# Kernel tuning notes

Measured on AMD Instinct MI355X. Metric: run time of the kernel, lower is better.

The kernel has to match this reference:

```python
import jax, jax.numpy as jnp
import numpy as np

N_NODES = 100000
N_EDGES = 3200000
IN_DIM, HID_DIM, LAT_DIM = 6, 32, 16


def gcn_conv(x, src, dst, W, b, num_nodes):
    """PyG-style GCNConv: add self-loops, symmetric deg^{-1/2} norm, linear, scatter-add.
    src/dst already include self-loops."""
    h = x @ W  # [N, out_dim] -- transform before propagate (small dims)
    ones = jnp.ones(src.shape[0], dtype=x.dtype)
    deg = jax.ops.segment_sum(ones, dst, num_segments=num_nodes)  # in-degree incl. self-loop
    dinv = jax.lax.rsqrt(jnp.maximum(deg, 1.0))
    norm = dinv[src] * dinv[dst]  # [E]
    msg = h[src] * norm[:, None]  # [E, out_dim] -- dominant memory traffic
    out = jax.ops.segment_sum(msg, dst, num_segments=num_nodes)
    return out + b


def setup_inputs() -> dict:
    key = jax.random.key(0)
    k1, k2, k3, k4 = jax.random.split(key, 4)
    x = jax.random.normal(k1, (N_NODES, IN_DIM), dtype=jnp.float32)
    edge_index = jax.random.randint(k2, (2, N_EDGES), 0, N_NODES, dtype=jnp.int64)
    # Glorot-ish init for weights, zeros for biases (PyG GCNConv defaults)
    W1 = jax.random.normal(k3, (IN_DIM, HID_DIM), dtype=jnp.float32) / np.sqrt(IN_DIM)
    b1 = jnp.zeros((HID_DIM,), dtype=jnp.float32)
    W2 = jax.random.normal(k4, (HID_DIM, LAT_DIM), dtype=jnp.float32) / np.sqrt(HID_DIM)
    b2 = jnp.zeros((LAT_DIM,), dtype=jnp.float32)
    return {"x": x, "edge_index": edge_index, "W1": W1, "b1": b1, "W2": W2, "b2": b2}


def reference(x, edge_index, W1, b1, W2, b2):
    num_nodes = x.shape[0]
    loops = jnp.arange(num_nodes, dtype=edge_index.dtype)
    src = jnp.concatenate([edge_index[0], loops])
    dst = jnp.concatenate([edge_index[1], loops])
    h = gcn_conv(x, src, dst, W1, b1, num_nodes)
    h = jax.nn.relu(h)
    # dropout is identity in eval mode (reference baseline)
    z = gcn_conv(h, src, dst, W2, b2, num_nodes)
    return z
```

## Files before the change

kernel.cpp:

```cpp
#include <hip/hip_runtime.h>
#include <hip/hip_fp16.h>

#define N_NODES 100000
#define N_EDGES 3200000
#define IN_DIM 6
#define HID_DIM 32
#define LAT_DIM 16

#define NPB 128
#define NB 782
#define CAP 4800
#define AB_BLOCKS 512
#define CH ((N_EDGES + AB_BLOCKS - 1) / AB_BLOCKS)
#define PL_T 512
#define LP2_CAP 2560

__global__ void k_init(int* __restrict__ bcur) {
    int i = blockIdx.x * blockDim.x + threadIdx.x;
    if (i < NB) bcur[i] = i * CAP;
}

__global__ void __launch_bounds__(PL_T) k_bplace(const int* __restrict__ src,
                                                 const int* __restrict__ dst,
                                                 int* __restrict__ bcur,
                                                 int* __restrict__ bedge, int E) {
    __shared__ int hist[NB];
    __shared__ int lbase[NB];
    __shared__ int gbase[NB];
    __shared__ int cur[NB];
    __shared__ int part[PL_T];
    __shared__ int stage[CH];
    __shared__ unsigned short sbkt[CH];
    int t = threadIdx.x;
    for (int i = t; i < NB; i += PL_T) { hist[i] = 0; cur[i] = 0; }
    __syncthreads();
    int beg = blockIdx.x * CH, end = min(beg + CH, E);
    int nv = (end - beg) >> 1;
    const int2* dst2 = (const int2*)(dst + beg);
    const long long* src2 = (const long long*)(src + beg);
    for (int i = t; i < nv; i += PL_T) {
        int2 d = dst2[i];
        atomicAdd(&hist[d.x >> 7], 1);
        atomicAdd(&hist[d.y >> 7], 1);
    }
    if (((end - beg) & 1) && t == 0) atomicAdd(&hist[dst[end - 1] >> 7], 1);
    __syncthreads();
    int i0 = 2 * t;
    int a = (i0 < NB) ? hist[i0] : 0;
    int b = (i0 + 1 < NB) ? hist[i0 + 1] : 0;
    part[t] = a + b;
    __syncthreads();
    for (int off = 1; off < PL_T; off <<= 1) {
        int v = (t >= off) ? part[t - off] : 0;
        __syncthreads();
        part[t] += v;
        __syncthreads();
    }
    int ex = (t == 0) ? 0 : part[t - 1];
    if (i0 < NB) lbase[i0] = ex;
    if (i0 + 1 < NB) lbase[i0 + 1] = ex + a;
    __syncthreads();
    for (int i = t; i < NB; i += PL_T)
        gbase[i] = hist[i] ? atomicAdd(&bcur[i], hist[i]) : 0;
    __syncthreads();
    for (int i = t; i < nv; i += PL_T) {
        int2 d = dst2[i];
        long long sv = __builtin_nontemporal_load(src2 + i);
        int s0 = (int)(sv & 0xFFFFFFFFLL);
        int s1 = (int)(sv >> 32);
        int bkt0 = d.x >> 7;
        int r0 = atomicAdd(&cur[bkt0], 1);
        int pos0 = lbase[bkt0] + r0;
        stage[pos0] = (s0 << 7) | (d.x & (NPB - 1));
        sbkt[pos0] = (unsigned short)bkt0;
        int bkt1 = d.y >> 7;
        int r1 = atomicAdd(&cur[bkt1], 1);
        int pos1 = lbase[bkt1] + r1;
        stage[pos1] = (s1 << 7) | (d.y & (NPB - 1));
        sbkt[pos1] = (unsigned short)bkt1;
    }
    if (((end - beg) & 1) && t == 0) {
        int d = dst[end - 1], s = src[end - 1];
        int bkt = d >> 7;
        int r = atomicAdd(&cur[bkt], 1);
        int pos = lbase[bkt] + r;
        stage[pos] = (s << 7) | (d & (NPB - 1));
        sbkt[pos] = (unsigned short)bkt;
    }
    __syncthreads();
    int total = end - beg;
    for (int j = t; j < total; j += PL_T) {
        int bkt = sbkt[j];
        bedge[gbase[bkt] + (j - lbase[bkt])] = stage[j];
    }
}

__global__ void __launch_bounds__(256) k_sort(const int* __restrict__ bcur,
                                              const int* __restrict__ bedge,
                                              const float* __restrict__ x,
                                              int2* __restrict__ rowse,
                                              int* __restrict__ perm,
                                              float* __restrict__ dinv,
                                              __half* __restrict__ xs, int N) {
    int b = blockIdx.x;
    __shared__ int cnt[NPB], base[NPB], cur[NPB], scn[NPB];
    __shared__ float dvs[NPB];
    __shared__ int pstage[CAP];
    int t = threadIdx.x;
    if (t < NPB) cnt[t] = 0;
    __syncthreads();
    int beg = b * CAP, end = bcur[b];
    int m = end - beg;
    for (int k = t; k < m; k += blockDim.x)
        atomicAdd(&cnt[bedge[beg + k] & (NPB - 1)], 1);
    __syncthreads();
    if (t < NPB) scn[t] = cnt[t];
    __syncthreads();
    for (int off = 1; off < NPB; off <<= 1) {
        int v = 0;
        if (t < NPB && t >= off) v = scn[t - off];
        __syncthreads();
        if (t < NPB) scn[t] += v;
        __syncthreads();
    }
    if (t < NPB) {
        int ex = scn[t] - cnt[t];
        base[t] = ex;
        cur[t] = 0;
        int node = (b << 7) + t;
        if (node < N) {
            float dv = rsqrtf((float)(cnt[t] + 1));
            dvs[t] = dv;
            dinv[node] = dv;
            rowse[node] = make_int2(beg + ex, beg + ex + cnt[t]);
        }
    }
    __syncthreads();
    for (int k = t; k < m; k += blockDim.x) {
        int w = bedge[beg + k];
        int dl = w & (NPB - 1);
        int pos = base[dl] + atomicAdd(&cur[dl], 1);
        pstage[pos] = w >> 7;
    }
    __syncthreads();
    for (int k = t; k < m; k += blockDim.x)
        perm[beg + k] = pstage[k];
    for (int i = t; i < NPB * 4; i += blockDim.x) {
        int nl = i >> 2, d2 = (i & 3) * 2;
        int node = (b << 7) + nl;
        if (node < N) {
            float dv = dvs[nl];
            float v0 = (d2 < IN_DIM) ? x[(size_t)node * IN_DIM + d2] * dv : 0.f;
            float v1 = (d2 + 1 < IN_DIM) ? x[(size_t)node * IN_DIM + d2 + 1] * dv : 0.f;
            *(__half2*)(xs + (size_t)node * 8 + d2) = __floats2half2_rn(v0, v1);
        }
    }
}

__global__ void __launch_bounds__(256) k_agg1f(const int2* __restrict__ rowse,
                                               const int* __restrict__ perm,
                                               const __half* __restrict__ xs,
                                               const float* __restrict__ dinv,
                                               const float* __restrict__ b1,
                                               const float* __restrict__ W1,
                                               const float* __restrict__ W2,
                                               __half* __restrict__ h2s, int N) {
    __shared__ float w1[IN_DIM * HID_DIM];
    __shared__ float w2[HID_DIM * LAT_DIM];
    __shared__ float bsh[HID_DIM];
    __shared__ float ash[64][HID_DIM + 1];
    __shared__ float y[64][9];
    __shared__ int lperm[LP2_CAP];
    int t = threadIdx.x;
    for (int i = t; i < IN_DIM * HID_DIM; i += 256) w1[i] = W1[i];
    for (int i = t; i < HID_DIM * LAT_DIM; i += 256) w2[i] = W2[i];
    if (t < HID_DIM) bsh[t] = b1[t];
    int nl = t >> 2, p = t & 3;
    int n0 = blockIdx.x * 64;
    int node = n0 + nl;
    int nlast = min(n0 + 63, N - 1);
    int gbeg = rowse[n0].x;
    int gend = rowse[nlast].y;
    int m = gend - gbeg;
    bool valid = (node <= nlast);
    int2 se = valid ? rowse[node] : make_int2(gbeg, gbeg);
    float2 acc = make_float2(0.f, 0.f);
    if (m <= LP2_CAP) {
        for (int i = t; i < m; i += 256) lperm[i] = perm[gbeg + i];
        __syncthreads();
        int k = se.x - gbeg, lend = se.y - gbeg;
        for (; k + 16 <= lend; k += 16) {
            int ss[16];
#pragma unroll
            for (int j = 0; j < 16; j++) ss[j] = lperm[k + j];
            __half2 gg[16];
#pragma unroll
            for (int j = 0; j < 16; j++)
                gg[j] = *(const __half2*)(xs + (size_t)ss[j] * 8 + p * 2);
            float px = 0.f, py = 0.f;
#pragma unroll
            for (int j = 0; j < 16; j++) {
                float2 f = __half22float2(gg[j]);
                px += f.x; py += f.y;
            }
            acc.x += px; acc.y += py;
        }
        for (; k < lend; ++k) {
            float2 f = __half22float2(*(const __half2*)(xs + (size_t)lperm[k] * 8 + p * 2));
            acc.x += f.x; acc.y += f.y;
        }
    } else {
        __syncthreads();
        for (int k = se.x; k < se.y; ++k) {
            float2 f = __half22float2(*(const __half2*)(xs + (size_t)perm[k] * 8 + p * 2));
            acc.x += f.x; acc.y += f.y;
        }
    }
    if (valid) {
        float2 f = __half22float2(*(const __half2*)(xs + (size_t)node * 8 + p * 2));
        y[nl][2 * p] = acc.x + f.x;
        y[nl][2 * p + 1] = acc.y + f.y;
    }
    __syncthreads();
    if (valid) {
        float dv = dinv[node];
        float yy[IN_DIM];
#pragma unroll
        for (int k2 = 0; k2 < IN_DIM; k2++) yy[k2] = y[nl][k2];
        int c0 = p * 8;
#pragma unroll
        for (int q = 0; q < 8; q++) {
            float z = 0.f;
#pragma unroll
            for (int k2 = 0; k2 < IN_DIM; k2++) z += yy[k2] * w1[k2 * HID_DIM + c0 + q];
            ash[nl][c0 + q] = fmaxf(dv * z + bsh[c0 + q], 0.f);
        }
    }
    __syncthreads();
    if (valid) {
        float dv = dinv[node];
        int c = p * 4;
        float z0 = 0.f, z1 = 0.f, z2 = 0.f, z3 = 0.f;
#pragma unroll
        for (int k2 = 0; k2 < HID_DIM; k2++) {
            float a = ash[nl][k2];
            z0 += a * w2[k2 * LAT_DIM + c];
            z1 += a * w2[k2 * LAT_DIM + c + 1];
            z2 += a * w2[k2 * LAT_DIM + c + 2];
            z3 += a * w2[k2 * LAT_DIM + c + 3];
        }
        __half2 h0 = __floats2half2_rn(dv * z0, dv * z1);
        __half2 h1 = __floats2half2_rn(dv * z2, dv * z3);
        uint2 u;
        u.x = *(unsigned*)&h0;
        u.y = *(unsigned*)&h1;
        *(uint2*)(h2s + (size_t)node * LAT_DIM + c) = u;
    }
}

__global__ void __launch_bounds__(256) k_agg2(const int2* __restrict__ rowse,
                                              const int* __restrict__ perm,
                                              const __half* __restrict__ h2s,
                                              const float* __restrict__ dinv,
                                              const float* __restrict__ b2,
                                              float* __restrict__ out, int N) {
    __shared__ int lperm[LP2_CAP];
    int t = threadIdx.x;
    int n0 = blockIdx.x * 64;
    int node = n0 + (t >> 2), p = t & 3;
    int nlast = min(n0 + 63, N - 1);
    int gbeg = rowse[n0].x;
    int gend = rowse[nlast].y;
    int m = gend - gbeg;
    int2 se = (node <= nlast) ? rowse[node] : make_int2(gbeg, gbeg);
    float4 acc = make_float4(0.f, 0.f, 0.f, 0.f);
    if (m <= LP2_CAP) {
        for (int i = t; i < m; i += 256) lperm[i] = perm[gbeg + i];
        __syncthreads();
        int k = se.x - gbeg, lend = se.y - gbeg;
        for (; k + 16 <= lend; k += 16) {
            int ss[16];
#pragma unroll
            for (int j = 0; j < 16; j++) ss[j] = lperm[k + j];
            uint2 gg[16];
#pragma unroll
            for (int j = 0; j < 16; j++)
                gg[j] = *(const uint2*)(h2s + (size_t)ss[j] * LAT_DIM + p * 4);
#pragma unroll
            for (int j = 0; j < 16; j++) {
                float2 f0 = __half22float2(*(const __half2*)&gg[j].x);
                float2 f1 = __half22float2(*(const __half2*)&gg[j].y);
                acc.x += f0.x; acc.y += f0.y; acc.z += f1.x; acc.w += f1.y;
            }
        }
        for (; k < lend; ++k) {
            uint2 g = *(const uint2*)(h2s + (size_t)lperm[k] * LAT_DIM + p * 4);
            float2 f0 = __half22float2(*(const __half2*)&g.x);
            float2 f1 = __half22float2(*(const __half2*)&g.y);
            acc.x += f0.x; acc.y += f0.y; acc.z += f1.x; acc.w += f1.y;
        }
    } else {
        __syncthreads();
        for (int k = se.x; k < se.y; ++k) {
            uint2 g = *(const uint2*)(h2s + (size_t)perm[k] * LAT_DIM + p * 4);
            float2 f0 = __half22float2(*(const __half2*)&g.x);
            float2 f1 = __half22float2(*(const __half2*)&g.y);
            acc.x += f0.x; acc.y += f0.y; acc.z += f1.x; acc.w += f1.y;
        }
    }
    if (node < N) {
        uint2 hh = *(const uint2*)(h2s + (size_t)node * LAT_DIM + p * 4);
        float2 h0 = __half22float2(*(const __half2*)&hh.x);
        float2 h1 = __half22float2(*(const __half2*)&hh.y);
        float dv = dinv[node];
        float4 bb = *(const float4*)(b2 + p * 4);
        float4 o;
        o.x = dv * (acc.x + h0.x) + bb.x;
        o.y = dv * (acc.y + h0.y) + bb.y;
        o.z = dv * (acc.z + h1.x) + bb.z;
        o.w = dv * (acc.w + h1.y) + bb.w;
        *(float4*)(out + (size_t)node * LAT_DIM + p * 4) = o;
    }
}

extern "C" void kernel_launch(void* const* d_in, const int* in_sizes, int n_in,
                              void* d_out, int out_size, void* d_ws, size_t ws_size,
                              hipStream_t stream) {
    const float* x  = (const float*)d_in[0];
    const int*   ei = (const int*)d_in[1];
    const float* W1 = (const float*)d_in[2];
    const float* b1 = (const float*)d_in[3];
    const float* W2 = (const float*)d_in[4];
    const float* b2 = (const float*)d_in[5];
    float* out = (float*)d_out;

    const int N = N_NODES, E = N_EDGES;
    const int* src = ei;
    const int* dst = ei + E;

    char* ws = (char*)d_ws;
    size_t off = 0;
    auto take = [&](size_t bytes) -> void* {
        void* p = ws + off;
        off += (bytes + 255) & ~(size_t)255;
        return p;
    };
    int*    bcur  = (int*)take((size_t)NB * 4);
    int*    bedge = (int*)take((size_t)NB * CAP * 4);
    int*    perm  = (int*)take((size_t)NB * CAP * 4);
    int2*   rowse = (int2*)take((size_t)N * 8);
    float*  dinv  = (float*)take((size_t)N * 4);
    __half* xs    = (__half*)take((size_t)N * 8 * 2);
    __half* h2s   = (__half*)take((size_t)N * LAT_DIM * 2);

    const int B = 256;
    k_init<<<(NB + B - 1) / B, B, 0, stream>>>(bcur);
    k_bplace<<<AB_BLOCKS, PL_T, 0, stream>>>(src, dst, bcur, bedge, E);
    k_sort<<<NB, B, 0, stream>>>(bcur, bedge, x, rowse, perm, dinv, xs, N);
    k_agg1f<<<(N + 63) / 64, B, 0, stream>>>(rowse, perm, xs, dinv, b1, W1, W2, h2s, N);
    k_agg2<<<(N + 63) / 64, B, 0, stream>>>(rowse, perm, h2s, dinv, b2, out, N);
}
```

Baseline: 103.4 us.

## Halve bucket width to 64 nodes and simplify bucket placement and sort

Buckets now hold 64 destination nodes instead of 128, which doubles the bucket count and gives the sort kernel twice as many smaller blocks. The per-bucket prefix scan is replaced by a single-wavefront shuffle scan. Placement reuses the histogram array for the global bases and folds the local cursor into pre-offset positions. The odd-tail handling is dropped on the assumption that the edge count divides evenly across blocks. Risks: the smaller CAP of 2560 per bucket could overflow if degrees are skewed, and the larger NB raises LDS use and histogram work in the placement kernel.

```diff
diff --git a/kernel.cpp b/kernel.cpp
--- a/kernel.cpp
+++ b/kernel.cpp
@@ -7,13 +7,13 @@
 #define HID_DIM 32
 #define LAT_DIM 16
 
-#define NPB 128
-#define NB 782
-#define CAP 4800
+#define NPB 64
+#define NB 1563
+#define CAP 2560
 #define AB_BLOCKS 512
-#define CH ((N_EDGES + AB_BLOCKS - 1) / AB_BLOCKS)
+#define CH (N_EDGES / AB_BLOCKS)
 #define PL_T 512
-#define LP2_CAP 2560
+#define LP2_CAP CAP
 
 __global__ void k_init(int* __restrict__ bcur) {
     int i = blockIdx.x * blockDim.x + threadIdx.x;
@@ -26,29 +26,29 @@
                                                  int* __restrict__ bedge, int E) {
     __shared__ int hist[NB];
     __shared__ int lbase[NB];
-    __shared__ int gbase[NB];
-    __shared__ int cur[NB];
+    __shared__ int curp[NB];
     __shared__ int part[PL_T];
     __shared__ int stage[CH];
     __shared__ unsigned short sbkt[CH];
     int t = threadIdx.x;
-    for (int i = t; i < NB; i += PL_T) { hist[i] = 0; cur[i] = 0; }
-    __syncthreads();
-    int beg = blockIdx.x * CH, end = min(beg + CH, E);
-    int nv = (end - beg) >> 1;
+    for (int i = t; i < NB; i += PL_T) hist[i] = 0;
+    __syncthreads();
+    int beg = blockIdx.x * CH;
+    int nv = CH >> 1;
     const int2* dst2 = (const int2*)(dst + beg);
     const long long* src2 = (const long long*)(src + beg);
     for (int i = t; i < nv; i += PL_T) {
         int2 d = dst2[i];
-        atomicAdd(&hist[d.x >> 7], 1);
-        atomicAdd(&hist[d.y >> 7], 1);
-    }
-    if (((end - beg) & 1) && t == 0) atomicAdd(&hist[dst[end - 1] >> 7], 1);
-    __syncthreads();
-    int i0 = 2 * t;
-    int a = (i0 < NB) ? hist[i0] : 0;
-    int b = (i0 + 1 < NB) ? hist[i0 + 1] : 0;
-    part[t] = a + b;
+        atomicAdd(&hist[d.x >> 6], 1);
+        atomicAdd(&hist[d.y >> 6], 1);
+    }
+    __syncthreads();
+    int i0 = 4 * t;
+    int a0 = (i0 < NB) ? hist[i0] : 0;
+    int a1 = (i0 + 1 < NB) ? hist[i0 + 1] : 0;
+    int a2 = (i0 + 2 < NB) ? hist[i0 + 2] : 0;
+    int a3 = (i0 + 3 < NB) ? hist[i0 + 3] : 0;
+    part[t] = a0 + a1 + a2 + a3;
     __syncthreads();
     for (int off = 1; off < PL_T; off <<= 1) {
         int v = (t >= off) ? part[t - off] : 0;
@@ -57,41 +57,34 @@
         __syncthreads();
     }
     int ex = (t == 0) ? 0 : part[t - 1];
-    if (i0 < NB) lbase[i0] = ex;
-    if (i0 + 1 < NB) lbase[i0 + 1] = ex + a;
-    __syncthreads();
-    for (int i = t; i < NB; i += PL_T)
-        gbase[i] = hist[i] ? atomicAdd(&bcur[i], hist[i]) : 0;
+    if (i0 < NB)     { lbase[i0]     = ex;              curp[i0]     = ex; }
+    if (i0 + 1 < NB) { lbase[i0 + 1] = ex + a0;         curp[i0 + 1] = ex + a0; }
+    if (i0 + 2 < NB) { lbase[i0 + 2] = ex + a0 + a1;    curp[i0 + 2] = ex + a0 + a1; }
+    if (i0 + 3 < NB) { lbase[i0 + 3] = ex + a0 + a1 + a2; curp[i0 + 3] = ex + a0 + a1 + a2; }
+    __syncthreads();
+    for (int i = t; i < NB; i += PL_T) {
+        int h = hist[i];
+        hist[i] = h ? atomicAdd(&bcur[i], h) : 0;
+    }
     __syncthreads();
     for (int i = t; i < nv; i += PL_T) {
         int2 d = dst2[i];
         long long sv = __builtin_nontemporal_load(src2 + i);
         int s0 = (int)(sv & 0xFFFFFFFFLL);
         int s1 = (int)(sv >> 32);
-        int bkt0 = d.x >> 7;
-        int r0 = atomicAdd(&cur[bkt0], 1);
-        int pos0 = lbase[bkt0] + r0;
-        stage[pos0] = (s0 << 7) | (d.x & (NPB - 1));
-        sbkt[pos0] = (unsigned short)bkt0;
-        int bkt1 = d.y >> 7;
-        int r1 = atomicAdd(&cur[bkt1], 1);
-        int pos1 = lbase[bkt1] + r1;
-        stage[pos1] = (s1 << 7) | (d.y & (NPB - 1));
-        sbkt[pos1] = (unsigned short)bkt1;
-    }
-    if (((end - beg) & 1) && t == 0) {
-        int d = dst[end - 1], s = src[end - 1];
-        int bkt = d >> 7;
-        int r = atomicAdd(&cur[bkt], 1);
-        int pos = lbase[bkt] + r;
-        stage[pos] = (s << 7) | (d & (NPB - 1));
-        sbkt[pos] = (unsigned short)bkt;
-    }
-    __syncthreads();
-    int total = end - beg;
-    for (int j = t; j < total; j += PL_T) {
+        int b0 = d.x >> 6;
+        int pos0 = atomicAdd(&curp[b0], 1);
+        stage[pos0] = (s0 << 6) | (d.x & (NPB - 1));
+        sbkt[pos0] = (unsigned short)b0;
+        int b1 = d.y >> 6;
+        int pos1 = atomicAdd(&curp[b1], 1);
+        stage[pos1] = (s1 << 6) | (d.y & (NPB - 1));
+        sbkt[pos1] = (unsigned short)b1;
+    }
+    __syncthreads();
+    for (int j = t; j < CH; j += PL_T) {
         int bkt = sbkt[j];
-        bedge[gbase[bkt] + (j - lbase[bkt])] = stage[j];
+        bedge[hist[bkt] + (j - lbase[bkt])] = stage[j];
     }
 }
 
@@ -103,7 +96,7 @@
                                               float* __restrict__ dinv,
                                               __half* __restrict__ xs, int N) {
     int b = blockIdx.x;
-    __shared__ int cnt[NPB], base[NPB], cur[NPB], scn[NPB];
+    __shared__ int cnt[NPB], cur[NPB];
     __shared__ float dvs[NPB];
     __shared__ int pstage[CAP];
     int t = threadIdx.x;
@@ -111,43 +104,39 @@
     __syncthreads();
     int beg = b * CAP, end = bcur[b];
     int m = end - beg;
-    for (int k = t; k < m; k += blockDim.x)
+    for (int k = t; k < m; k += 256)
         atomicAdd(&cnt[bedge[beg + k] & (NPB - 1)], 1);
     __syncthreads();
-    if (t < NPB) scn[t] = cnt[t];
-    __syncthreads();
-    for (int off = 1; off < NPB; off <<= 1) {
-        int v = 0;
-        if (t < NPB && t >= off) v = scn[t - off];
-        __syncthreads();
-        if (t < NPB) scn[t] += v;
-        __syncthreads();
-    }
-    if (t < NPB) {
-        int ex = scn[t] - cnt[t];
-        base[t] = ex;
-        cur[t] = 0;
-        int node = (b << 7) + t;
+    if (t < 64) {
+        int c = cnt[t];
+        int xv = c;
+#pragma unroll
+        for (int off = 1; off < 64; off <<= 1) {
+            int v = __shfl_up(xv, off);
+            if (t >= off) xv += v;
+        }
+        int ex = xv - c;
+        cur[t] = ex;
+        int node = (b << 6) + t;
         if (node < N) {
-            float dv = rsqrtf((float)(cnt[t] + 1));
+            float dv = rsqrtf((float)(c + 1));
             dvs[t] = dv;
             dinv[node] = dv;
-            rowse[node] = make_int2(beg + ex, beg + ex + cnt[t]);
-        }
-    }
-    __syncthreads();
-    for (int k = t; k < m; k += blockDim.x) {
+            rowse[node] = make_int2(beg + ex, beg + ex + c);
+        }
+    }
+    __syncthreads();
+    for (int k = t; k < m; k += 256) {
         int w = bedge[beg + k];
-        int dl = w & (NPB - 1);
-        int pos = base[dl] + atomicAdd(&cur[dl], 1);
-        pstage[pos] = w >> 7;
-    }
-    __syncthreads();
-    for (int k = t; k < m; k += blockDim.x)
+        int pos = atomicAdd(&cur[w & (NPB - 1)], 1);
+        pstage[pos] = w >> 6;
+    }
+    __syncthreads();
+    for (int k = t; k < m; k += 256)
         perm[beg + k] = pstage[k];
-    for (int i = t; i < NPB * 4; i += blockDim.x) {
-        int nl = i >> 2, d2 = (i & 3) * 2;
-        int node = (b << 7) + nl;
+    {
+        int nl = t >> 2, d2 = (t & 3) * 2;
+        int node = (b << 6) + nl;
         if (node < N) {
             float dv = dvs[nl];
             float v0 = (d2 < IN_DIM) ? x[(size_t)node * IN_DIM + d2] * dv : 0.f;
@@ -357,6 +346,6 @@
     k_init<<<(NB + B - 1) / B, B, 0, stream>>>(bcur);
     k_bplace<<<AB_BLOCKS, PL_T, 0, stream>>>(src, dst, bcur, bedge, E);
     k_sort<<<NB, B, 0, stream>>>(bcur, bedge, x, rowse, perm, dinv, xs, N);
-    k_agg1f<<<(N + 63) / 64, B, 0, stream>>>(rowse, perm, xs, dinv, b1, W1, W2, h2s, N);
-    k_agg2<<<(N + 63) / 64, B, 0, stream>>>(rowse, perm, h2s, dinv, b2, out, N);
-}
+    k_agg1f<<<NB, B, 0, stream>>>(rowse, perm, xs, dinv, b1, W1, W2, h2s, N);
+    k_agg2<<<NB, B, 0, stream>>>(rowse, perm, h2s, dinv, b2, out, N);
+}
```

Result: slower. 106.7 us (+3.2%).
